# Optimization experiments

Hardware: AMD Instinct MI355X
Metric: run time of the kernel (lower is better)

## Reference

```python
import jax, jax.numpy as jnp
import numpy as np

B, H, W, C = 4, 256, 256, 64
KH = KW = 3
UNITS = 1          # forced: conv in-channels must equal kernel in-channels (see notes)
G = 1              # num_deformable_group
HP, WP = H + 2, W + 2  # 'same' padding for 3x3 stride-1: pad 1 each side


def _conv_indices(h, w):
    """Replicates tf.image.extract_image_patches('SAME') on an index grid:
    border patches read zero-padded coordinates. Returns int [h, w, 9]."""
    yg, xg = jnp.meshgrid(jnp.arange(h), jnp.arange(w), indexing='ij')
    yp = jnp.pad(yg, 1)
    xp = jnp.pad(xg, 1)
    ys = jnp.stack([yp[ky:ky + h, kx:kx + w] for ky in range(KH) for kx in range(KW)], -1)
    xs = jnp.stack([xp[ky:ky + h, kx:kx + w] for ky in range(KH) for kx in range(KW)], -1)
    return ys, xs


def setup_inputs() -> dict:
    key = jax.random.key(0)
    k1, k2, k3, k4 = jax.random.split(key, 4)
    input_fp = jax.random.normal(k1, (B, H, W, C), jnp.float32)
    gt_mask = jax.random.randint(k2, (1, H, W, 1), 0, 2).astype(jnp.float32)
    offset = jax.random.normal(k3, (B, H, W, UNITS * KH * KW * 2), jnp.float32)
    fan_in = KH * KW * C
    kernel = jax.random.normal(k4, (KH, KW, C, UNITS), jnp.float32) / np.float32(np.sqrt(fan_in))
    bias = jnp.zeros((UNITS,), jnp.float32)
    return {"input_fp": input_fp, "gt_mask": gt_mask, "offset": offset,
            "kernel": kernel, "bias": bias}


def reference(input_fp, gt_mask, offset, kernel, bias):
    pad = ((0, 0), (1, 1), (1, 1), (0, 0))
    fp = jnp.pad(input_fp, pad)                 # [B, HP, WP, C]
    mk = jnp.pad(gt_mask, pad)[0, :, :, 0]      # [HP, WP]; original tiles this over batch/channels

    off = offset.reshape(B, H, W, UNITS * KH * KW, 2)
    y_off, x_off = off[..., 0], off[..., 1]     # [B, H, W, 9]

    yi, xi = _conv_indices(H, W)                # [H, W, 9] int
    yf = yi[None].astype(jnp.float32)           # [1, H, W, 9], broadcasts over batch
    xf = xi[None].astype(jnp.float32)

    # mask at base sample points and at offset sample points
    p_mask = mk[yi, xi][None]                                        # [1, H, W, 9]
    yo = jnp.clip(jnp.floor(yf + y_off).astype(jnp.int32), 0, HP - 1)
    xo = jnp.clip(jnp.floor(xf + x_off).astype(jnp.int32), 0, WP - 1)
    p_mask_off = mk[yo, xo]                                          # [B, H, W, 9]
    diff = (p_mask != p_mask_off).astype(jnp.float32)

    y = jnp.clip(yf + y_off * diff, 0.0, H - 1.0)
    x = jnp.clip(xf + x_off * diff, 0.0, W - 1.0)
    y0 = jnp.floor(y).astype(jnp.int32)
    x0 = jnp.floor(x).astype(jnp.int32)

    b = jnp.arange(B)[:, None, None, None]
    pixels = fp[b, y0, x0]                      # [B, H, W, 9, C] nearest-floor sampling
    # [B,H,W,kh,kw,G,C] -> [B,H,kh,W,kw,G,C] -> [B, H*kh, W*kw, G*C]
    pixels = pixels.reshape(B, H, W, KH, KW, G, C)
    pixels = pixels.transpose(0, 1, 3, 2, 4, 5, 6)
    pixels = pixels.reshape(B, H * KH, W * KW, G * C)   # feat_in_group = units//G = 1, tile is a no-op

    out = jax.lax.conv_general_dilated(
        pixels, kernel, window_strides=(KH, KW), padding='SAME',
        dimension_numbers=('NHWC', 'HWIO', 'NHWC'))      # [B, H, W, UNITS]
    return out + bias
```

## Files before the change

kernel.cpp:

```cpp
#include <hip/hip_runtime.h>

#define HW 256
#define CH 64
#define NPIX (4 * HW * HW)
#define DM_BYTES ((size_t)NPIX * 48)

__global__ __launch_bounds__(256, 8) void DeformD_kernel(
    const float* __restrict__ inp,
    const float* __restrict__ ker,
    float* __restrict__ dm)
{
    __shared__ float wlds[576];
    const int tid = threadIdx.x;
    if (tid < 144) ((float4*)wlds)[tid] = ((const float4*)ker)[tid];
    const float4* wq = (const float4*)wlds;

    const int lane = tid & 63;
    const int wave = tid >> 6;
    const int t = lane & 15;
    const int g = lane >> 4;

    const int p0 = blockIdx.x * 32 + (wave * 4 + g) * 2;

    const float4 v0 = *(const float4*)(inp + (size_t)p0 * 64 + t * 4);
    const float4 v1 = *(const float4*)(inp + (size_t)(p0 + 1) * 64 + t * 4);

    __syncthreads();

    float da[9], db[9];
    #pragma unroll
    for (int k = 0; k < 9; ++k) {
        const float4 w = wq[k * 16 + t];
        da[k] = v0.x * w.x + v0.y * w.y + v0.z * w.z + v0.w * w.w;
        db[k] = v1.x * w.x + v1.y * w.y + v1.z * w.z + v1.w * w.w;
    }
    #pragma unroll
    for (int k = 0; k < 9; ++k) {
        da[k] += __shfl_xor(da[k], 8);
        da[k] += __shfl_xor(da[k], 4);
        da[k] += __shfl_xor(da[k], 2);
        da[k] += __shfl_xor(da[k], 1);
        db[k] += __shfl_xor(db[k], 8);
        db[k] += __shfl_xor(db[k], 4);
        db[k] += __shfl_xor(db[k], 2);
        db[k] += __shfl_xor(db[k], 1);
    }
    float sa = da[8], sb = db[8];
    #pragma unroll
    for (int k = 7; k >= 0; --k) {
        sa = (t == k) ? da[k] : sa;
        sb = (t == k) ? db[k] : sb;
    }
    if (t < 9) {
        dm[(size_t)p0 * 12 + t] = sa;
        dm[(size_t)(p0 + 1) * 12 + t] = sb;
    }
}

__global__ __launch_bounds__(256, 4) void DeformC_kernel(
    const float* __restrict__ gt,
    const float* __restrict__ off,
    const float* __restrict__ dm,
    const float* __restrict__ bias,
    float* __restrict__ out)
{
    const int tid = threadIdx.x;
    const int bid = blockIdx.x;
    const int vb = (bid & 7) * 128 + (bid >> 3);
    const int p = vb * 256 + tid;
    const int b = p >> 16;
    const int i = (p >> 8) & 255;
    const int j = p & 255;

    const float* offp = off + (size_t)p * 18;
    float2 o[9];
    #pragma unroll
    for (int tap = 0; tap < 9; ++tap)
        o[tap] = *(const float2*)(offp + 2 * tap);

    const float* dmb = dm + (size_t)(b << 16) * 12;

    float sum = 0.f;
    #pragma unroll
    for (int tap = 0; tap < 9; ++tap) {
        const int ky = tap / 3, kx = tap - ky * 3;
        const int iy = i + ky - 1, ix = j + kx - 1;
        const bool interior = (iy >= 0) & (iy < HW) & (ix >= 0) & (ix < HW);
        const int yi = interior ? iy : 0;
        const int xi = interior ? ix : 0;
        const float p_mask = (yi >= 1 && xi >= 1) ? gt[(yi - 1) * HW + (xi - 1)] : 0.f;

        const float yf = (float)yi, xf = (float)xi;
        const float yof = fminf(fmaxf(floorf(yf + o[tap].x), 0.f), 257.f);
        const float xof = fminf(fmaxf(floorf(xf + o[tap].y), 0.f), 257.f);
        const int yo = (int)yof, xo = (int)xof;
        const float p_mask_off = (yo >= 1 && yo <= HW && xo >= 1 && xo <= HW)
                                 ? gt[(yo - 1) * HW + (xo - 1)] : 0.f;
        const float diff = (p_mask != p_mask_off) ? 1.f : 0.f;
        const float y = fminf(fmaxf(yf + o[tap].x * diff, 0.f), 255.f);
        const float x = fminf(fmaxf(xf + o[tap].y * diff, 0.f), 255.f);
        const int y0 = (int)y, x0 = (int)x;
        const bool valid = (y0 >= 1) & (x0 >= 1);
        const int idx = valid ? ((y0 - 1) * HW + (x0 - 1)) : 0;
        const float dval = dmb[(size_t)idx * 12 + tap];
        sum += valid ? dval : 0.f;
    }
    out[p] = sum + bias[0];
}

__global__ __launch_bounds__(256, 6) void DeformFallback_kernel(
    const float* __restrict__ inp, const float* __restrict__ gt,
    const float* __restrict__ off, const float* __restrict__ ker,
    const float* __restrict__ bias, float* __restrict__ out)
{
    __shared__ float wlds[576];
    const int tid = threadIdx.x;
    if (tid < 144) ((float4*)wlds)[tid] = ((const float4*)ker)[tid];

    const int lane = tid & 63;
    const int wave = tid >> 6;
    const int q16  = lane & 48;
    const int t    = lane & 15;

    const int bid = blockIdx.x;
    const int vb  = (bid & 7) * 2048 + (bid >> 3);

    const int p = vb * 16 + wave * 4 + (q16 >> 4);
    const int b = p >> 16;
    const int i = (p >> 8) & 255;
    const int j = p & 255;
    const float* inb = inp + (long)b * (HW * HW * CH);

    int pack = 0;
    if (t < 9) {
        const int tap = t;
        const int ky = tap / 3, kx = tap - ky * 3;
        int iy = i + ky - 1, ix = j + kx - 1;
        bool interior = (iy >= 0) & (iy < HW) & (ix >= 0) & (ix < HW);
        int yi = interior ? iy : 0;
        int xi = interior ? ix : 0;
        float p_mask = (yi >= 1 && xi >= 1) ? gt[(yi - 1) * HW + (xi - 1)] : 0.f;
        float2 o2 = *(const float2*)(off + (long)p * 18 + 2 * tap);
        float yf = (float)yi, xf = (float)xi;
        float yof = fminf(fmaxf(floorf(yf + o2.x), 0.f), 257.f);
        float xof = fminf(fmaxf(floorf(xf + o2.y), 0.f), 257.f);
        int yo = (int)yof, xo = (int)xof;
        float p_mask_off = (yo >= 1 && yo <= HW && xo >= 1 && xo <= HW)
                           ? gt[(yo - 1) * HW + (xo - 1)] : 0.f;
        float diff = (p_mask != p_mask_off) ? 1.f : 0.f;
        float y = fminf(fmaxf(yf + o2.x * diff, 0.f), 255.f);
        float x = fminf(fmaxf(xf + o2.y * diff, 0.f), 255.f);
        int y0 = (int)y;
        int x0 = (int)x;
        bool valid = (y0 >= 1) & (x0 >= 1);
        int eoff = ((y0 - 1) * HW + (x0 - 1)) * CH;
        pack = valid ? eoff : -1;
    }

    int pk[9];
    #pragma unroll
    for (int k = 0; k < 9; ++k) pk[k] = __shfl(pack, q16 + k);

    float4 v[9];
    #pragma unroll
    for (int k = 0; k < 9; ++k) {
        int eo2 = pk[k] >= 0 ? pk[k] : 0;
        v[k] = *(const float4*)(inb + eo2 + t * 4);
    }

    __syncthreads();

    float acc = 0.f;
    #pragma unroll
    for (int k = 0; k < 9; ++k) {
        float s = pk[k] >= 0 ? 1.f : 0.f;
        float4 w = ((const float4*)wlds)[k * 16 + t];
        float d = v[k].x * w.x + v[k].y * w.y + v[k].z * w.z + v[k].w * w.w;
        acc = fmaf(s, d, acc);
    }

    acc += __shfl_xor(acc, 8);
    acc += __shfl_xor(acc, 4);
    acc += __shfl_xor(acc, 2);
    acc += __shfl_xor(acc, 1);
    if (t == 0) out[p] = acc + bias[0];
}

extern "C" void kernel_launch(void* const* d_in, const int* in_sizes, int n_in,
                              void* d_out, int out_size, void* d_ws, size_t ws_size,
                              hipStream_t stream) {
    const float* inp  = (const float*)d_in[0];
    const float* gt   = (const float*)d_in[1];
    const float* off  = (const float*)d_in[2];
    const float* ker  = (const float*)d_in[3];
    const float* bias = (const float*)d_in[4];
    float* out = (float*)d_out;

    if (d_ws != nullptr && ws_size >= DM_BYTES) {
        DeformD_kernel<<<8192, 256, 0, stream>>>(inp, ker, (float*)d_ws);
        DeformC_kernel<<<1024, 256, 0, stream>>>(gt, off, (const float*)d_ws, bias, out);
    } else {
        DeformFallback_kernel<<<16384, 256, 0, stream>>>(inp, gt, off, ker, bias, out);
    }
}
```

Measured before the change: 135.3 us.

## Split offset/mask index computation into separate kernel with packed 16-bit encodings

Adds a kernel, run one thread per (pixel, tap), that computes the mask-gated sample coordinates and stores them as packed 16-bit y/x codes in the workspace. The gather kernel then reads 24 bytes of codes per pixel instead of 72 bytes of offsets plus mask lookups, and issues its nine dot-product gathers independently, allowing higher occupancy. The cost is an extra launch and an extra write and read of the encoded array, and the workspace requirement grows.

```diff
diff --git a/kernel.cpp b/kernel.cpp
--- a/kernel.cpp
+++ b/kernel.cpp
@@ -3,7 +3,44 @@
 #define HW 256
 #define CH 64
 #define NPIX (4 * HW * HW)
+#define ENC_BYTES ((size_t)NPIX * 24)
+#define DM_OFF ((size_t)8 << 20)
 #define DM_BYTES ((size_t)NPIX * 48)
+#define WS_NEED (DM_OFF + DM_BYTES)
+
+__global__ __launch_bounds__(256, 8) void DeformA_kernel(
+    const float* __restrict__ gt,
+    const float* __restrict__ off,
+    unsigned short* __restrict__ enc)
+{
+    const unsigned g = blockIdx.x * 256u + threadIdx.x;
+    const unsigned p = g / 9u;
+    const int tap = (int)(g - p * 9u);
+    const int i = (int)((p >> 8) & 255u);
+    const int j = (int)(p & 255u);
+    const int ky = tap / 3, kx = tap - ky * 3;
+
+    const float2 o2 = *(const float2*)(off + (size_t)g * 2);
+
+    const int iy = i + ky - 1, ix = j + kx - 1;
+    const bool interior = (iy >= 0) & (iy < HW) & (ix >= 0) & (ix < HW);
+    const int yi = interior ? iy : 0;
+    const int xi = interior ? ix : 0;
+    const float p_mask = (yi >= 1 && xi >= 1) ? gt[(yi - 1) * HW + (xi - 1)] : 0.f;
+
+    const float yf = (float)yi, xf = (float)xi;
+    const float yof = fminf(fmaxf(floorf(yf + o2.x), 0.f), 257.f);
+    const float xof = fminf(fmaxf(floorf(xf + o2.y), 0.f), 257.f);
+    const int yo = (int)yof, xo = (int)xof;
+    const float p_mask_off = (yo >= 1 && yo <= HW && xo >= 1 && xo <= HW)
+                             ? gt[(yo - 1) * HW + (xo - 1)] : 0.f;
+    const float diff = (p_mask != p_mask_off) ? 1.f : 0.f;
+    const float y = fminf(fmaxf(yf + o2.x * diff, 0.f), 255.f);
+    const float x = fminf(fmaxf(xf + o2.y * diff, 0.f), 255.f);
+    const int y0 = (int)y, x0 = (int)x;
+
+    enc[p * 12u + (unsigned)tap] = (unsigned short)((y0 << 8) | x0);
+}
 
 __global__ __launch_bounds__(256, 8) void DeformD_kernel(
     const float* __restrict__ inp,
@@ -57,9 +94,8 @@
     }
 }
 
-__global__ __launch_bounds__(256, 4) void DeformC_kernel(
-    const float* __restrict__ gt,
-    const float* __restrict__ off,
+__global__ __launch_bounds__(256, 8) void DeformC2_kernel(
+    const unsigned short* __restrict__ enc,
     const float* __restrict__ dm,
     const float* __restrict__ bias,
     float* __restrict__ out)
@@ -69,42 +105,36 @@
     const int vb = (bid & 7) * 128 + (bid >> 3);
     const int p = vb * 256 + tid;
     const int b = p >> 16;
-    const int i = (p >> 8) & 255;
-    const int j = p & 255;
-
-    const float* offp = off + (size_t)p * 18;
-    float2 o[9];
-    #pragma unroll
-    for (int tap = 0; tap < 9; ++tap)
-        o[tap] = *(const float2*)(offp + 2 * tap);
-
     const float* dmb = dm + (size_t)(b << 16) * 12;
 
+    const uint2* e = (const uint2*)(enc + (size_t)p * 12u);
+    const uint2 eA = e[0];
+    const uint2 eB = e[1];
+    const unsigned eC = *(const unsigned*)(e + 2);
+
+    unsigned en[9];
+    en[0] = eA.x & 0xffffu; en[1] = eA.x >> 16;
+    en[2] = eA.y & 0xffffu; en[3] = eA.y >> 16;
+    en[4] = eB.x & 0xffffu; en[5] = eB.x >> 16;
+    en[6] = eB.y & 0xffffu; en[7] = eB.y >> 16;
+    en[8] = eC & 0xffffu;
+
+    float v[9];
+    int msk = 0;
+    #pragma unroll
+    for (int k = 0; k < 9; ++k) {
+        const int yy = (int)(en[k] >> 8);
+        const int xx = (int)(en[k] & 255u);
+        const bool valid = (yy >= 1) & (xx >= 1);
+        msk |= (int)valid << k;
+        const int idx = valid ? ((yy - 1) * HW + (xx - 1)) : 0;
+        v[k] = dmb[(size_t)idx * 12 + k];
+    }
     float sum = 0.f;
     #pragma unroll
-    for (int tap = 0; tap < 9; ++tap) {
-        const int ky = tap / 3, kx = tap - ky * 3;
-        const int iy = i + ky - 1, ix = j + kx - 1;
-        const bool interior = (iy >= 0) & (iy < HW) & (ix >= 0) & (ix < HW);
-        const int yi = interior ? iy : 0;
-        const int xi = interior ? ix : 0;
-        const float p_mask = (yi >= 1 && xi >= 1) ? gt[(yi - 1) * HW + (xi - 1)] : 0.f;
-
-        const float yf = (float)yi, xf = (float)xi;
-        const float yof = fminf(fmaxf(floorf(yf + o[tap].x), 0.f), 257.f);
-        const float xof = fminf(fmaxf(floorf(xf + o[tap].y), 0.f), 257.f);
-        const int yo = (int)yof, xo = (int)xof;
-        const float p_mask_off = (yo >= 1 && yo <= HW && xo >= 1 && xo <= HW)
-                                 ? gt[(yo - 1) * HW + (xo - 1)] : 0.f;
-        const float diff = (p_mask != p_mask_off) ? 1.f : 0.f;
-        const float y = fminf(fmaxf(yf + o[tap].x * diff, 0.f), 255.f);
-        const float x = fminf(fmaxf(xf + o[tap].y * diff, 0.f), 255.f);
-        const int y0 = (int)y, x0 = (int)x;
-        const bool valid = (y0 >= 1) & (x0 >= 1);
-        const int idx = valid ? ((y0 - 1) * HW + (x0 - 1)) : 0;
-        const float dval = dmb[(size_t)idx * 12 + tap];
-        sum += valid ? dval : 0.f;
-    }
+    for (int k = 0; k < 9; ++k)
+        sum += ((msk >> k) & 1) ? v[k] : 0.f;
+
     out[p] = sum + bias[0];
 }
 
@@ -196,9 +226,12 @@
     const float* bias = (const float*)d_in[4];
     float* out = (float*)d_out;
 
-    if (d_ws != nullptr && ws_size >= DM_BYTES) {
-        DeformD_kernel<<<8192, 256, 0, stream>>>(inp, ker, (float*)d_ws);
-        DeformC_kernel<<<1024, 256, 0, stream>>>(gt, off, (const float*)d_ws, bias, out);
+    if (d_ws != nullptr && ws_size >= WS_NEED) {
+        unsigned short* enc = (unsigned short*)d_ws;
+        float* dm = (float*)((char*)d_ws + DM_OFF);
+        DeformA_kernel<<<9216, 256, 0, stream>>>(gt, off, enc);
+        DeformD_kernel<<<8192, 256, 0, stream>>>(inp, ker, dm);
+        DeformC2_kernel<<<1024, 256, 0, stream>>>(enc, dm, bias, out);
     } else {
         DeformFallback_kernel<<<16384, 256, 0, stream>>>(inp, gt, off, ker, bias, out);
     }
```

New measurement: 138.8 us. 1.03x slower.
